# Optimization experiments

Measured on AMD Instinct MI355X. Metric: run time of the kernel, lower is better.

The kernel has to match this reference:

```python
import jax, jax.numpy as jnp
import numpy as np

N_HEAD = 16


def setup_inputs() -> dict:
    key = jax.random.key(0)
    k1, k2, k3 = jax.random.split(key, 3)
    B, T, C = 2, 2048, 1024
    x = jax.random.normal(k1, (B, T, C), dtype=jnp.float32)
    w_attn = jax.random.normal(k2, (C, 3 * C), dtype=jnp.float32) * 0.02
    w_proj = jax.random.normal(k3, (C, C), dtype=jnp.float32) * 0.02
    return {"x": x, "w_attn": w_attn, "w_proj": w_proj}


def reference(x, w_attn, w_proj):
    B, T, C = x.shape
    H = N_HEAD
    D = C // H
    qkv = x @ w_attn  # [B, T, 3C]
    q, k, v = jnp.split(qkv, 3, axis=2)
    q = q.reshape(B, T, H, D)
    k = k.reshape(B, T, H, D)
    v = v.reshape(B, T, H, D)
    scale = 1.0 / jnp.sqrt(jnp.asarray(D, dtype=x.dtype))
    # Full T x T score matrix, matching the 'standard_attention' path.
    att = jnp.einsum('bthd,bshd->bhts', q, k) * scale  # [B, H, T, T]
    causal = jnp.tril(jnp.ones((T, T), dtype=bool))
    att = jnp.where(causal[None, None, :, :], att, jnp.asarray(-jnp.inf, dtype=att.dtype))
    att = jax.nn.softmax(att, axis=-1)
    # dropout_p is False (== 0.0) in the original module, so no dropout applied.
    y = jnp.einsum('bhts,bshd->bthd', att, v)  # [B, T, H, D]
    y = y.reshape(B, T, C)
    return y @ w_proj
```

## Files before the change

### kernel.cpp

```cpp
#include <hip/hip_runtime.h>
#include <hip/hip_bf16.h>
#include <math.h>

#define BB 2
#define TT 2048
#define HH 16
#define DD 64
#define CC 1024
#define C3 3072

typedef __attribute__((ext_vector_type(8))) short bf16x8;
typedef __attribute__((ext_vector_type(4))) short bf16x4;
typedef __attribute__((ext_vector_type(4))) float f32x4;
typedef __attribute__((ext_vector_type(2))) unsigned int u32x2;

__device__ __forceinline__ unsigned short f2bf(float f) {
  union { float f; unsigned u; } v; v.f = f;
  unsigned r = v.u + 0x7fffu + ((v.u >> 16) & 1u);
  return (unsigned short)(r >> 16);
}
__device__ __forceinline__ unsigned pack2bf(float a, float b) {
  __hip_bfloat162 h = __float22bfloat162_rn(make_float2(a, b));
  union { __hip_bfloat162 h; unsigned u; } cv; cv.h = h;
  return cv.u;
}

__device__ __forceinline__ void async_cp16(const void* g, void* l) {
  __builtin_amdgcn_global_load_lds(
      (const __attribute__((address_space(1))) void*)g,
      (__attribute__((address_space(3))) void*)l, 16, 0, 0);
}

__global__ __launch_bounds__(256)
void prep(const float* __restrict__ x, const float* __restrict__ w_attn,
          const float* __restrict__ w_proj, unsigned short* __restrict__ xb,
          unsigned short* __restrict__ wat, unsigned short* __restrict__ wpt) {
  __shared__ __align__(16) float Ts[64][68];
  const int bx = blockIdx.x, tid = threadIdx.x;
  if (bx < 1024) {
    int i = bx * 256 + tid;
#pragma unroll
    for (int it = 0; it < 4; ++it, i += 262144) {
      const float4 v = ((const float4*)x)[i];
      bf16x4 o = {(short)f2bf(v.x), (short)f2bf(v.y),
                  (short)f2bf(v.z), (short)f2bf(v.w)};
      ((bf16x4*)xb)[i] = o;
    }
    return;
  }
  const float* W;
  unsigned short* WT;
  int Nd, bound, n0, k0;
  float s;
  if (bx < 1792) {
    const int bid = bx - 1024;
    W = w_attn; WT = wat; Nd = 3072; bound = 1024; s = 0.18033688f;
    n0 = (bid % 48) * 64; k0 = (bid / 48) * 64;
  } else {
    const int bid = bx - 1792;
    W = w_proj; WT = wpt; Nd = 1024; bound = 0; s = 1.0f;
    n0 = (bid % 16) * 64; k0 = (bid / 16) * 64;
  }
  const int rl = tid >> 4, c4 = tid & 15;
#pragma unroll
  for (int it = 0; it < 4; ++it) {
    const int r = it * 16 + rl;
    *(float4*)&Ts[r][c4 * 4] =
        *(const float4*)(W + (size_t)(k0 + r) * Nd + n0 + c4 * 4);
  }
  __syncthreads();
#pragma unroll
  for (int it = 0; it < 4; ++it) {
    const int n = it * 16 + rl;
    const float sc = (n0 + n < bound) ? s : 1.0f;
    bf16x4 o = {(short)f2bf(Ts[c4 * 4 + 0][n] * sc),
                (short)f2bf(Ts[c4 * 4 + 1][n] * sc),
                (short)f2bf(Ts[c4 * 4 + 2][n] * sc),
                (short)f2bf(Ts[c4 * 4 + 3][n] * sc)};
    *(bf16x4*)(WT + (size_t)(n0 + n) * CC + k0 + c4 * 4) = o;
  }
}

__global__ __launch_bounds__(256, 3)
void gemm_qkv(const unsigned short* __restrict__ A,
              const unsigned short* __restrict__ BT,
              unsigned short* __restrict__ Cb,
              unsigned short* __restrict__ Vout) {
  __shared__ __align__(16) unsigned short As[2 * 128 * 32];
  __shared__ __align__(16) unsigned short Bs[2 * 128 * 32];

  const int tid = threadIdx.x;
  const int w = tid >> 6, lane = tid & 63;
  const int l15 = lane & 15, quad = lane >> 4;
  const int wm = w >> 1, wn = w & 1;
  const int row0 = blockIdx.y * 128, col0 = blockIdx.x * 128;

  const int ca0 = tid, ca1 = tid + 256;
  const int ra0 = ca0 >> 2, ka0 = ((ca0 & 3) ^ ((ca0 >> 3) & 3)) * 8;
  const int ra1 = ca1 >> 2, ka1 = ((ca1 & 3) ^ ((ca1 >> 3) & 3)) * 8;
  const unsigned short* gA0 = A + (size_t)(row0 + ra0) * CC + ka0;
  const unsigned short* gA1 = A + (size_t)(row0 + ra1) * CC + ka1;
  const unsigned short* gB0 = BT + (size_t)(col0 + ra0) * CC + ka0;
  const unsigned short* gB1 = BT + (size_t)(col0 + ra1) * CC + ka1;
  const int la0 = tid * 16, la1 = tid * 16 + 4096;

  const int fro = l15 * 64 + 16 * (quad ^ ((l15 >> 1) & 3));

  f32x4 acc[4][4];
#pragma unroll
  for (int i = 0; i < 4; ++i)
#pragma unroll
    for (int j = 0; j < 4; ++j) acc[i][j] = (f32x4){0.f, 0.f, 0.f, 0.f};

  async_cp16(gA0, (char*)As + la0);
  async_cp16(gA1, (char*)As + la1);
  async_cp16(gB0, (char*)Bs + la0);
  async_cp16(gB1, (char*)Bs + la1);

  for (int i = 0; i < 32; ++i) {
    const int cur = i & 1;
    __syncthreads();

    if (i + 1 < 32) {
      const int k1 = (i + 1) * 32;
      const int ab = (cur ^ 1) * 8192;
      async_cp16(gA0 + k1, (char*)As + ab + la0);
      async_cp16(gA1 + k1, (char*)As + ab + la1);
      async_cp16(gB0 + k1, (char*)Bs + ab + la0);
      async_cp16(gB1 + k1, (char*)Bs + ab + la1);
    }

    const char* fA = (const char*)As + cur * 8192 + wm * 4096 + fro;
    const char* fB = (const char*)Bs + cur * 8192 + wn * 4096 + fro;

    bf16x8 af[4], bf[4];
#pragma unroll
    for (int mt = 0; mt < 4; ++mt) af[mt] = *(const bf16x8*)(fA + mt * 1024);
#pragma unroll
    for (int nt = 0; nt < 4; ++nt) bf[nt] = *(const bf16x8*)(fB + nt * 1024);
#pragma unroll
    for (int mt = 0; mt < 4; ++mt)
#pragma unroll
      for (int nt = 0; nt < 4; ++nt)
        acc[mt][nt] = __builtin_amdgcn_mfma_f32_16x16x32_bf16(
            af[mt], bf[nt], acc[mt][nt], 0, 0, 0);
  }

  if (col0 >= 2048) {
#pragma unroll
    for (int mt = 0; mt < 4; ++mt) {
      const int rbase = row0 + wm * 64 + mt * 16 + quad * 4;
      const int bq = rbase >> 11, t0 = rbase & 2047;
#pragma unroll
      for (int nt = 0; nt < 4; ++nt) {
        const int d = col0 + wn * 64 + nt * 16 + l15 - 2048;
        bf16x4 o = {(short)f2bf(acc[mt][nt][0]), (short)f2bf(acc[mt][nt][1]),
                    (short)f2bf(acc[mt][nt][2]), (short)f2bf(acc[mt][nt][3])};
        *(bf16x4*)(Vout + (((size_t)(bq << 10) + d) << 11) + t0) = o;
      }
    }
  } else {
#pragma unroll
    for (int mt = 0; mt < 4; ++mt) {
      const int rbase = row0 + wm * 64 + mt * 16 + quad * 4;
#pragma unroll
      for (int r = 0; r < 4; ++r) {
        unsigned short* cr =
            Cb + (size_t)(rbase + r) * C3 + col0 + wn * 64 + l15;
#pragma unroll
        for (int nt = 0; nt < 4; ++nt) cr[nt * 16] = f2bf(acc[mt][nt][r]);
      }
    }
  }
}

__global__ __launch_bounds__(256, 2)
void gemm_out(const unsigned short* __restrict__ A,
              const unsigned short* __restrict__ BT,
              float* __restrict__ Cf) {
  __shared__ __align__(16) unsigned short As[2 * 64 * 64];
  __shared__ __align__(16) unsigned short Bs[2 * 128 * 64];

  const int tid = threadIdx.x;
  const int w = tid >> 6, lane = tid & 63;
  const int l15 = lane & 15, quad = lane >> 4;
  const int wm = w >> 1, wn = w & 1;
  const int row0 = blockIdx.y * 64, col0 = blockIdx.x * 128;

  const int ca0 = tid, ca1 = tid + 256;
  const int ra0 = ca0 >> 3, ka0 = ((ca0 & 7) ^ ((ca0 >> 3) & 7)) * 8;
  const int ra1 = ca1 >> 3, ka1 = ((ca1 & 7) ^ ((ca1 >> 3) & 7)) * 8;
  const unsigned short* gA0 = A + (size_t)(row0 + ra0) * CC + ka0;
  const unsigned short* gA1 = A + (size_t)(row0 + ra1) * CC + ka1;
  const unsigned short* gB[4];
  int lb[4];
#pragma unroll
  for (int t = 0; t < 4; ++t) {
    const int c = tid + t * 256;
    const int rb = c >> 3, kb = ((c & 7) ^ ((c >> 3) & 7)) * 8;
    gB[t] = BT + (size_t)(col0 + rb) * CC + kb;
    lb[t] = c * 16;
  }
  const int la0 = tid * 16, la1 = tid * 16 + 4096;

  const int fro = l15 * 128 + ((quad ^ (l15 & 7)) << 4);

  f32x4 acc[2][4];
#pragma unroll
  for (int i = 0; i < 2; ++i)
#pragma unroll
    for (int j = 0; j < 4; ++j) acc[i][j] = (f32x4){0.f, 0.f, 0.f, 0.f};

  async_cp16(gA0, (char*)As + la0);
  async_cp16(gA1, (char*)As + la1);
#pragma unroll
  for (int t = 0; t < 4; ++t) async_cp16(gB[t], (char*)Bs + lb[t]);

  for (int i = 0; i < 16; ++i) {
    const int cur = i & 1;
    __syncthreads();

    if (i + 1 < 16) {
      const int k1 = (i + 1) * 64;
      const int ab = (cur ^ 1) * 8192, bb = (cur ^ 1) * 16384;
      async_cp16(gA0 + k1, (char*)As + ab + la0);
      async_cp16(gA1 + k1, (char*)As + ab + la1);
#pragma unroll
      for (int t = 0; t < 4; ++t) async_cp16(gB[t] + k1, (char*)Bs + bb + lb[t]);
    }

    const char* fA = (const char*)As + cur * 8192 + wm * 4096 + fro;
    const char* fB = (const char*)Bs + cur * 16384 + wn * 8192 + fro;

#pragma unroll
    for (int kh = 0; kh < 2; ++kh) {
      const int xo = kh * 64;
      bf16x8 af[2], bf[4];
#pragma unroll
      for (int mt = 0; mt < 2; ++mt)
        af[mt] = *(const bf16x8*)(fA + mt * 2048 + ((fro + xo) & 127) - (fro & 127));
#pragma unroll
      for (int nt = 0; nt < 4; ++nt)
        bf[nt] = *(const bf16x8*)(fB + nt * 2048 + ((fro + xo) & 127) - (fro & 127));
#pragma unroll
      for (int mt = 0; mt < 2; ++mt)
#pragma unroll
        for (int nt = 0; nt < 4; ++nt)
          acc[mt][nt] = __builtin_amdgcn_mfma_f32_16x16x32_bf16(
              af[mt], bf[nt], acc[mt][nt], 0, 0, 0);
    }
  }

#pragma unroll
  for (int mt = 0; mt < 2; ++mt) {
    const int rbase = row0 + wm * 32 + mt * 16 + quad * 4;
#pragma unroll
    for (int r = 0; r < 4; ++r) {
      float* cr = Cf + (size_t)(rbase + r) * CC + col0 + wn * 64 + l15;
#pragma unroll
      for (int nt = 0; nt < 4; ++nt) cr[nt * 16] = acc[mt][nt][r];
    }
  }
}

__device__ __forceinline__ void s_exp_store(
    const int c, const int qt, const int l15, const int quad,
    const bf16x8 (&kf)[2][2], const bf16x8 (&qf)[4][2],
    char* psw, const int psrow, float (&lsum)[4]) {
#pragma unroll
  for (int ks = 0; ks < 2; ++ks)
#pragma unroll
    for (int qs = 0; qs < 4; ++qs) {
      f32x4 z = (f32x4){-12.f, -12.f, -12.f, -12.f};
      z = __builtin_amdgcn_mfma_f32_16x16x32_bf16(kf[ks][0], qf[qs][0], z, 0, 0, 0);
      z = __builtin_amdgcn_mfma_f32_16x16x32_bf16(kf[ks][1], qf[qs][1], z, 0, 0, 0);
      if (c >= 2 * qt) {
#pragma unroll
        for (int r = 0; r < 4; ++r)
          if (32 * c + ks * 16 + quad * 4 + r > qt * 64 + qs * 16 + l15)
            z[r] = -INFINITY;
      }
      u32x2 d;
      d[0] = pack2bf(__builtin_amdgcn_exp2f(z[0]),
                     __builtin_amdgcn_exp2f(z[1]));
      d[1] = pack2bf(__builtin_amdgcn_exp2f(z[2]),
                     __builtin_amdgcn_exp2f(z[3]));
      lsum[qs] += __uint_as_float(d[0] << 16) +
                  __uint_as_float(d[0] & 0xffff0000u) +
                  __uint_as_float(d[1] << 16) +
                  __uint_as_float(d[1] & 0xffff0000u);
      *(u32x2*)(psw + qs * 2304 + psrow + (((ks + l15) & 3) << 5) + quad * 8) = d;
    }
}

__device__ __forceinline__ void pv_accum(
    const int l15, const int quad, const bf16x8 (&vf)[4],
    const char* psw, const int psrow, f32x4 (&O)[4][4]) {
  __builtin_amdgcn_s_setprio(1);
#pragma unroll
  for (int qs = 0; qs < 4; ++qs) {
    const bf16x8 pf = *(const bf16x8*)(psw + qs * 2304 + psrow +
                                       ((((quad >> 1) + l15) & 3) << 5) +
                                       ((quad & 1) << 4));
#pragma unroll
    for (int dt = 0; dt < 4; ++dt)
      O[dt][qs] = __builtin_amdgcn_mfma_f32_16x16x32_bf16(vf[dt], pf, O[dt][qs], 0, 0, 0);
  }
  __builtin_amdgcn_s_setprio(0);
}

#define LOADK_P(dst, kp)                                                 \
  do {                                                                   \
    dst[0][0] = *(const bf16x8*)(kp);                                    \
    dst[0][1] = *(const bf16x8*)((kp) + 32);                             \
    dst[1][0] = *(const bf16x8*)((kp) + 16 * C3);                        \
    dst[1][1] = *(const bf16x8*)((kp) + 16 * C3 + 32);                   \
  } while (0)

#define LOADV_P(dst, vp)                                                 \
  do {                                                                   \
    dst[0] = *(const bf16x8*)(vp);                                       \
    dst[1] = *(const bf16x8*)((vp) + 16 * TT);                           \
    dst[2] = *(const bf16x8*)((vp) + 32 * TT);                           \
    dst[3] = *(const bf16x8*)((vp) + 48 * TT);                           \
  } while (0)

__global__ __launch_bounds__(256, 3)
void attn_mfma(const unsigned short* __restrict__ qkvb,
               const unsigned short* __restrict__ vt,
               unsigned short* __restrict__ y) {
  const int n = blockIdx.x;
  const int bh = (n & 7) + 8 * ((n >> 3) & 3);
  const int qt = 31 - (n >> 5);
  const int b = bh >> 4, h = bh & 15;
  const int tid = threadIdx.x;
  const int w = tid >> 6;
  const int lane = tid & 63;
  const int l15 = lane & 15, quad = lane >> 4;

  __shared__ __align__(16) char arena[36864];
  __shared__ float Red2[2][4][16];

  char* psw = arena + w * 9216;
  const int psrow = l15 * 144;
  const int epoff = l15 * 64 + ((quad ^ (l15 & 3)) << 4);

  const int nc = 2 * (qt + 1);

  const unsigned short* kbase =
      qkvb + (size_t)(b * TT + l15) * C3 + 1024 + h * DD + quad * 8;
  const unsigned short* vbase =
      vt + (size_t)(bh * DD + l15) * TT + quad * 8;

  const unsigned short* qbase =
      qkvb + (size_t)(b * TT + qt * 64 + l15) * C3 + h * DD + quad * 8;
  bf16x8 qf[4][2];
#pragma unroll
  for (int qs = 0; qs < 4; ++qs)
#pragma unroll
    for (int kh = 0; kh < 2; ++kh)
      qf[qs][kh] = *(const bf16x8*)(qbase + qs * 16 * C3 + kh * 32);

  f32x4 O[4][4];
  float lsum[4] = {0.f, 0.f, 0.f, 0.f};
#pragma unroll
  for (int dt = 0; dt < 4; ++dt)
#pragma unroll
    for (int qs = 0; qs < 4; ++qs) O[dt][qs] = (f32x4){0.f, 0.f, 0.f, 0.f};

  int c = w;
  if (c < nc) {
    const unsigned short* kp = kbase + (size_t)(32 * c) * C3;
    const unsigned short* vp = vbase + 32 * c;
    bf16x8 kf[2][2], vf[4];
    LOADK_P(kf, kp);
    LOADV_P(vf, vp);
    while (c + 4 < nc) {
      s_exp_store(c, qt, l15, quad, kf, qf, psw, psrow, lsum);
      kp += (size_t)128 * C3;
      LOADK_P(kf, kp);
      pv_accum(l15, quad, vf, psw, psrow, O);
      vp += 128;
      LOADV_P(vf, vp);
      c += 4;
    }
    s_exp_store(c, qt, l15, quad, kf, qf, psw, psrow, lsum);
    pv_accum(l15, quad, vf, psw, psrow, O);
  }

#pragma unroll
  for (int qs = 0; qs < 4; ++qs) {
    lsum[qs] += __shfl_xor(lsum[qs], 16, 64);
    lsum[qs] += __shfl_xor(lsum[qs], 32, 64);
  }

  __syncthreads();
  if (w & 1) {
    char* rs = arena + (w >> 1) * 16384;
#pragma unroll
    for (int dt = 0; dt < 4; ++dt)
#pragma unroll
      for (int qs = 0; qs < 4; ++qs)
        *(f32x4*)(rs + (dt * 4 + qs) * 1024 + epoff) = O[dt][qs];
    if (quad == 0) {
#pragma unroll
      for (int qs = 0; qs < 4; ++qs) Red2[w >> 1][qs][l15] = lsum[qs];
    }
  }
  __syncthreads();
  if (!(w & 1)) {
    char* rs = arena + (w >> 1) * 16384;
#pragma unroll
    for (int dt = 0; dt < 4; ++dt)
#pragma unroll
      for (int qs = 0; qs < 4; ++qs)
        O[dt][qs] += *(const f32x4*)(rs + (dt * 4 + qs) * 1024 + epoff);
#pragma unroll
    for (int qs = 0; qs < 4; ++qs) lsum[qs] += Red2[w >> 1][qs][l15];
  }
  __syncthreads();
  if (w == 2) {
    char* rs = arena;
#pragma unroll
    for (int dt = 0; dt < 4; ++dt)
#pragma unroll
      for (int qs = 0; qs < 4; ++qs)
        *(f32x4*)(rs + (dt * 4 + qs) * 1024 + epoff) = O[dt][qs];
    if (quad == 0) {
#pragma unroll
      for (int qs = 0; qs < 4; ++qs) Red2[0][qs][l15] = lsum[qs];
    }
  }
  __syncthreads();
  if (w == 0) {
    const char* rs = arena;
#pragma unroll
    for (int dt = 0; dt < 4; ++dt)
#pragma unroll
      for (int qs = 0; qs < 4; ++qs)
        O[dt][qs] += *(const f32x4*)(rs + (dt * 4 + qs) * 1024 + epoff);
    unsigned short* yr =
        y + (size_t)(b * TT + qt * 64 + l15) * CC + h * DD + quad * 4;
#pragma unroll
    for (int qs = 0; qs < 4; ++qs) {
      const float inv = 1.0f / (lsum[qs] + Red2[0][qs][l15]);
#pragma unroll
      for (int dt = 0; dt < 4; ++dt) {
        bf16x4 o = {(short)f2bf(O[dt][qs][0] * inv),
                    (short)f2bf(O[dt][qs][1] * inv),
                    (short)f2bf(O[dt][qs][2] * inv),
                    (short)f2bf(O[dt][qs][3] * inv)};
        *(bf16x4*)(yr + (size_t)qs * 16 * CC + dt * 16) = o;
      }
    }
  }
}

extern "C" void kernel_launch(void* const* d_in, const int* in_sizes, int n_in,
                              void* d_out, int out_size, void* d_ws,
                              size_t ws_size, hipStream_t stream) {
  const float* x      = (const float*)d_in[0];
  const float* w_attn = (const float*)d_in[1];
  const float* w_proj = (const float*)d_in[2];
  float* out = (float*)d_out;

  unsigned short* xb   = (unsigned short*)d_ws;
  unsigned short* wat  = xb + (size_t)4096 * 1024;
  unsigned short* wpt  = wat + (size_t)3072 * 1024;
  unsigned short* qkvb = wpt + (size_t)1024 * 1024;
  unsigned short* vt   = qkvb + (size_t)4096 * 3072;
  unsigned short* yb   = vt + (size_t)BB * HH * DD * TT;

  dim3 blk(256);

  prep<<<2048, blk, 0, stream>>>(x, w_attn, w_proj, xb, wat, wpt);

  gemm_qkv<<<dim3(C3 / 128, (BB * TT) / 128), blk, 0, stream>>>(
      xb, wat, qkvb, vt);

  attn_mfma<<<dim3(1024, 1, 1), blk, 0, stream>>>(qkvb, vt, yb);

  gemm_out<<<dim3(CC / 128, (BB * TT) / 64), blk, 0, stream>>>(yb, wpt, out);
}
```

Baseline: 195.3 us.

## Split attention warps into query-half pairs and interleave causal tile scheduling

Each 64-query block now assigns two warps to each 32-query half, and the two warps in a pair split the key chunks between them. This replaces the four-way key split over all 64 queries. Per-warp state (O, lsum, Q fragments) and LDS use are halved, the final reduction shrinks from two levels to one, and causal masking skips key chunks beyond each half's diagonal. The block-to-query-tile mapping also changes from strictly descending to an interleaved order, to balance the uneven causal work across the grid. Each warp now reads twice as many K/V chunks relative to its MFMA work, so global traffic per block rises.

Measured after the change: 198.1 us. About the same (+1.4%).

```diff
diff --git a/kernel.cpp b/kernel.cpp
--- a/kernel.cpp
+++ b/kernel.cpp
@@ -263,21 +263,22 @@
   }
 }
 
-__device__ __forceinline__ void s_exp_store(
-    const int c, const int qt, const int l15, const int quad,
-    const bf16x8 (&kf)[2][2], const bf16x8 (&qf)[4][2],
-    char* psw, const int psrow, float (&lsum)[4]) {
+__device__ __forceinline__ void s_exp_store2(
+    const int c, const int qt, const int qh, const int l15, const int quad,
+    const bf16x8 (&kf)[2][2], const bf16x8 (&qf)[2][2],
+    char* psw, const int psrow, float (&lsum)[2]) {
 #pragma unroll
   for (int ks = 0; ks < 2; ++ks)
 #pragma unroll
-    for (int qs = 0; qs < 4; ++qs) {
+    for (int qs = 0; qs < 2; ++qs) {
       f32x4 z = (f32x4){-12.f, -12.f, -12.f, -12.f};
       z = __builtin_amdgcn_mfma_f32_16x16x32_bf16(kf[ks][0], qf[qs][0], z, 0, 0, 0);
       z = __builtin_amdgcn_mfma_f32_16x16x32_bf16(kf[ks][1], qf[qs][1], z, 0, 0, 0);
-      if (c >= 2 * qt) {
+      if (c >= 2 * qt + qh) {
 #pragma unroll
         for (int r = 0; r < 4; ++r)
-          if (32 * c + ks * 16 + quad * 4 + r > qt * 64 + qs * 16 + l15)
+          if (32 * c + ks * 16 + quad * 4 + r >
+              qt * 64 + qh * 32 + qs * 16 + l15)
             z[r] = -INFINITY;
       }
       u32x2 d;
@@ -293,12 +294,12 @@
     }
 }
 
-__device__ __forceinline__ void pv_accum(
+__device__ __forceinline__ void pv_accum2(
     const int l15, const int quad, const bf16x8 (&vf)[4],
-    const char* psw, const int psrow, f32x4 (&O)[4][4]) {
+    const char* psw, const int psrow, f32x4 (&O)[4][2]) {
   __builtin_amdgcn_s_setprio(1);
 #pragma unroll
-  for (int qs = 0; qs < 4; ++qs) {
+  for (int qs = 0; qs < 2; ++qs) {
     const bf16x8 pf = *(const bf16x8*)(psw + qs * 2304 + psrow +
                                        ((((quad >> 1) + l15) & 3) << 5) +
                                        ((quad & 1) << 4));
@@ -331,21 +332,20 @@
                unsigned short* __restrict__ y) {
   const int n = blockIdx.x;
   const int bh = (n & 7) + 8 * ((n >> 3) & 3);
-  const int qt = 31 - (n >> 5);
+  const int m = n >> 5, p = m & 7, g = m >> 3;
+  const int qt = (g == 0) ? p : (g == 1) ? 31 - p : (g == 2) ? 15 - p : 16 + p;
   const int b = bh >> 4, h = bh & 15;
   const int tid = threadIdx.x;
-  const int w = tid >> 6;
-  const int lane = tid & 63;
+  const int w = tid >> 6, lane = tid & 63;
   const int l15 = lane & 15, quad = lane >> 4;
-
-  __shared__ __align__(16) char arena[36864];
-  __shared__ float Red2[2][4][16];
-
-  char* psw = arena + w * 9216;
+  const int qh = w >> 1, kp2 = w & 1;
+
+  __shared__ __align__(16) char arena[18432];
+  __shared__ float Red2[2][2][16];
+
+  char* psw = arena + w * 4608;
   const int psrow = l15 * 144;
   const int epoff = l15 * 64 + ((quad ^ (l15 & 3)) << 4);
-
-  const int nc = 2 * (qt + 1);
 
   const unsigned short* kbase =
       qkvb + (size_t)(b * TT + l15) * C3 + 1024 + h * DD + quad * 8;
@@ -353,97 +353,74 @@
       vt + (size_t)(bh * DD + l15) * TT + quad * 8;
 
   const unsigned short* qbase =
-      qkvb + (size_t)(b * TT + qt * 64 + l15) * C3 + h * DD + quad * 8;
-  bf16x8 qf[4][2];
-#pragma unroll
-  for (int qs = 0; qs < 4; ++qs)
+      qkvb + (size_t)(b * TT + qt * 64 + qh * 32 + l15) * C3 + h * DD + quad * 8;
+  bf16x8 qf[2][2];
+#pragma unroll
+  for (int qs = 0; qs < 2; ++qs)
 #pragma unroll
     for (int kh = 0; kh < 2; ++kh)
       qf[qs][kh] = *(const bf16x8*)(qbase + qs * 16 * C3 + kh * 32);
 
-  f32x4 O[4][4];
-  float lsum[4] = {0.f, 0.f, 0.f, 0.f};
+  f32x4 O[4][2];
+  float lsum[2] = {0.f, 0.f};
 #pragma unroll
   for (int dt = 0; dt < 4; ++dt)
 #pragma unroll
-    for (int qs = 0; qs < 4; ++qs) O[dt][qs] = (f32x4){0.f, 0.f, 0.f, 0.f};
-
-  int c = w;
-  if (c < nc) {
+    for (int qs = 0; qs < 2; ++qs) O[dt][qs] = (f32x4){0.f, 0.f, 0.f, 0.f};
+
+  const int cl = 2 * qt + qh;
+  int c = kp2;
+  if (c <= cl) {
     const unsigned short* kp = kbase + (size_t)(32 * c) * C3;
     const unsigned short* vp = vbase + 32 * c;
     bf16x8 kf[2][2], vf[4];
     LOADK_P(kf, kp);
     LOADV_P(vf, vp);
-    while (c + 4 < nc) {
-      s_exp_store(c, qt, l15, quad, kf, qf, psw, psrow, lsum);
-      kp += (size_t)128 * C3;
+    while (c + 2 <= cl) {
+      s_exp_store2(c, qt, qh, l15, quad, kf, qf, psw, psrow, lsum);
+      kp += (size_t)64 * C3;
       LOADK_P(kf, kp);
-      pv_accum(l15, quad, vf, psw, psrow, O);
-      vp += 128;
+      pv_accum2(l15, quad, vf, psw, psrow, O);
+      vp += 64;
       LOADV_P(vf, vp);
-      c += 4;
-    }
-    s_exp_store(c, qt, l15, quad, kf, qf, psw, psrow, lsum);
-    pv_accum(l15, quad, vf, psw, psrow, O);
-  }
-
-#pragma unroll
-  for (int qs = 0; qs < 4; ++qs) {
+      c += 2;
+    }
+    s_exp_store2(c, qt, qh, l15, quad, kf, qf, psw, psrow, lsum);
+    pv_accum2(l15, quad, vf, psw, psrow, O);
+  }
+
+#pragma unroll
+  for (int qs = 0; qs < 2; ++qs) {
     lsum[qs] += __shfl_xor(lsum[qs], 16, 64);
     lsum[qs] += __shfl_xor(lsum[qs], 32, 64);
   }
 
   __syncthreads();
-  if (w & 1) {
-    char* rs = arena + (w >> 1) * 16384;
+  if (kp2) {
+    char* rs = arena + qh * 8192;
 #pragma unroll
     for (int dt = 0; dt < 4; ++dt)
 #pragma unroll
-      for (int qs = 0; qs < 4; ++qs)
-        *(f32x4*)(rs + (dt * 4 + qs) * 1024 + epoff) = O[dt][qs];
+      for (int qs = 0; qs < 2; ++qs)
+        *(f32x4*)(rs + (dt * 2 + qs) * 1024 + epoff) = O[dt][qs];
     if (quad == 0) {
 #pragma unroll
-      for (int qs = 0; qs < 4; ++qs) Red2[w >> 1][qs][l15] = lsum[qs];
+      for (int qs = 0; qs < 2; ++qs) Red2[qh][qs][l15] = lsum[qs];
     }
   }
   __syncthreads();
-  if (!(w & 1)) {
-    char* rs = arena + (w >> 1) * 16384;
+  if (!kp2) {
+    const char* rs = arena + qh * 8192;
 #pragma unroll
     for (int dt = 0; dt < 4; ++dt)
 #pragma unroll
-      for (int qs = 0; qs < 4; ++qs)
-        O[dt][qs] += *(const f32x4*)(rs + (dt * 4 + qs) * 1024 + epoff);
-#pragma unroll
-    for (int qs = 0; qs < 4; ++qs) lsum[qs] += Red2[w >> 1][qs][l15];
-  }
-  __syncthreads();
-  if (w == 2) {
-    char* rs = arena;
-#pragma unroll
-    for (int dt = 0; dt < 4; ++dt)
-#pragma unroll
-      for (int qs = 0; qs < 4; ++qs)
-        *(f32x4*)(rs + (dt * 4 + qs) * 1024 + epoff) = O[dt][qs];
-    if (quad == 0) {
-#pragma unroll
-      for (int qs = 0; qs < 4; ++qs) Red2[0][qs][l15] = lsum[qs];
-    }
-  }
-  __syncthreads();
-  if (w == 0) {
-    const char* rs = arena;
-#pragma unroll
-    for (int dt = 0; dt < 4; ++dt)
-#pragma unroll
-      for (int qs = 0; qs < 4; ++qs)
-        O[dt][qs] += *(const f32x4*)(rs + (dt * 4 + qs) * 1024 + epoff);
+      for (int qs = 0; qs < 2; ++qs)
+        O[dt][qs] += *(const f32x4*)(rs + (dt * 2 + qs) * 1024 + epoff);
     unsigned short* yr =
-        y + (size_t)(b * TT + qt * 64 + l15) * CC + h * DD + quad * 4;
-#pragma unroll
-    for (int qs = 0; qs < 4; ++qs) {
-      const float inv = 1.0f / (lsum[qs] + Red2[0][qs][l15]);
+        y + (size_t)(b * TT + qt * 64 + qh * 32 + l15) * CC + h * DD + quad * 4;
+#pragma unroll
+    for (int qs = 0; qs < 2; ++qs) {
+      const float inv = 1.0f / (lsum[qs] + Red2[qh][qs][l15]);
 #pragma unroll
       for (int dt = 0; dt < 4; ++dt) {
         bf16x4 o = {(short)f2bf(O[dt][qs][0] * inv),
```
